# Kernel tuning notes

Measured on AMD Instinct MI355X. Metric: run time of the kernel, lower is better.

The kernel has to match this reference:

```python
import jax, jax.numpy as jnp
import numpy as np

T, B, F, H, P = 256, 512, 256, 512, 12  # seq len, batch, feature_dim, hidden_dim, p_interval


def setup_inputs() -> dict:
    key = jax.random.key(0)
    ks = jax.random.split(key, 9)
    s = 1.0 / np.sqrt(F + H)  # torch Linear default init scale
    def lin(k):
        kw, kb = jax.random.split(k)
        W = jax.random.uniform(kw, (F + H, H), jnp.float32, -s, s)
        b = jax.random.uniform(kb, (H,), jnp.float32, -s, s)
        return W, b
    Wf, bf = lin(ks[0])
    Wi, bi = lin(ks[1])
    Wo, bo = lin(ks[2])
    Wg, bg = lin(ks[3])
    x = jax.random.normal(ks[4], (T, B, F), jnp.float32)
    return {"x": x, "Wf": Wf, "bf": bf, "Wi": Wi, "bi": bi,
            "Wo": Wo, "bo": bo, "Wg": Wg, "bg": bg}


def _slstm(x, Wf, bf, Wi, bi, Wo, bo, Wg, bg):
    Tn, Bn, _ = x.shape
    h0 = jnp.zeros((P, Bn, H), x.dtype)
    # NOTE: original torch code reassigns c to a 2D [B,H] tensor after step 0,
    # so c[t % P] indexes a batch ROW (shape [H]) that broadcasts. At t=0 the
    # slice is all-zeros either way, so carrying a 2D c is exactly faithful.
    c0 = jnp.zeros((Bn, H), x.dtype)

    def step(carry, inp):
        h, c = carry
        x_t, t = inp
        idx = t % P
        xc = jnp.concatenate([x_t, h[idx]], axis=1)  # [B, F+H]
        f = jax.nn.softmax(xc @ Wf + bf, axis=1)
        i = jax.nn.softmax(xc @ Wi + bi, axis=1)
        o = jax.nn.softmax(xc @ Wo + bo, axis=1)
        g = jnp.tanh(xc @ Wg + bg)
        c_new = jnp.tanh(f * c[idx] + i * g)  # c[idx]: row [H], broadcasts over B
        h = h.at[idx].set(o * c_new)
        return (h, c_new), None

    (h, _), _ = jax.lax.scan(step, (h0, c0), (x, jnp.arange(Tn)))
    return h[(Tn - 1) % P]


def reference(x, Wf, bf, Wi, bi, Wo, bo, Wg, bg):
    return _slstm(x, Wf, bf, Wi, bi, Wo, bo, Wg, bg)
```

## Files before the change

kernel.cpp:

```cpp
#include <hip/hip_runtime.h>

typedef unsigned short u16;
typedef unsigned int   u32;

typedef __attribute__((ext_vector_type(8))) short bf16x8;
typedef __attribute__((ext_vector_type(16))) float f32x16;

__device__ __forceinline__ u16 f2bf(float v) {
    u32 u = __float_as_uint(v);
    u32 r = (u + 0x7fffu + ((u >> 16) & 1u)) >> 16;
    return (u16)r;
}
__device__ __forceinline__ float bf2f(u16 h) { return __uint_as_float(((u32)h) << 16); }

__device__ __forceinline__ float ftanh(float x) {
    float e = __expf(2.0f * x);
    return 1.0f - 2.0f * __builtin_amdgcn_rcpf(e + 1.0f);
}

__device__ __forceinline__ void gl2lds16(const void* g, void* l) {
    __builtin_amdgcn_global_load_lds(
        (const __attribute__((address_space(1))) void*)g,
        (__attribute__((address_space(3))) void*)l, 16, 0, 0);
}

__global__ void init_k(u16* __restrict__ hh, u16* __restrict__ hl, float* __restrict__ cb) {
    int i = blockIdx.x * 256 + threadIdx.x;
    hh[i] = 0; hl[i] = 0;
    if (i < 2 * 512) cb[i] = 0.0f;
}

__global__ void pack_wq(const float* __restrict__ Wf, const float* __restrict__ bf_,
                        const float* __restrict__ Wi, const float* __restrict__ bi_,
                        const float* __restrict__ Wo, const float* __restrict__ bo_,
                        const float* __restrict__ Wg, const float* __restrict__ bg_,
                        u16* __restrict__ wq, float* __restrict__ bias4) {
    int idx = blockIdx.x * 256 + threadIdx.x;
    int n = idx / 768, k = idx - n * 768;
    int gate = n >> 9, col = n & 511;
    const float* W = (gate == 0) ? Wf : (gate == 1) ? Wi : (gate == 2) ? Wo : Wg;
    float v = W[k * 512 + col];
    u16 h = f2bf(v);
    u16 l = f2bf(v - bf2f(h));
    size_t base = (size_t)n * 2304;
    if (k < 256) {
        wq[base + k] = h; wq[base + 512 + k] = h; wq[base + 256 + k] = l;
    } else {
        int d = k - 256;
        wq[base + 768 + d] = h; wq[base + 1792 + d] = h; wq[base + 1280 + d] = l;
    }
    if (k == 0) {
        const float* bb = (gate == 0) ? bf_ : (gate == 1) ? bi_ : (gate == 2) ? bo_ : bg_;
        bias4[n] = bb[col];
    }
}

__global__ void split_x(const float* __restrict__ src, u16* __restrict__ oh, u16* __restrict__ ol) {
    int i = blockIdx.x * 256 + threadIdx.x;
    float4 v = ((const float4*)src)[i];
    u16 hx = f2bf(v.x), hy = f2bf(v.y), hz = f2bf(v.z), hw = f2bf(v.w);
    u16 lx = f2bf(v.x - bf2f(hx)), ly = f2bf(v.y - bf2f(hy));
    u16 lz = f2bf(v.z - bf2f(hz)), lw = f2bf(v.w - bf2f(hw));
    uint2 hv; hv.x = (u32)hx | ((u32)hy << 16); hv.y = (u32)hz | ((u32)hw << 16);
    uint2 lv; lv.x = (u32)lx | ((u32)ly << 16); lv.y = (u32)lz | ((u32)lw << 16);
    ((uint2*)oh)[i] = hv;
    ((uint2*)ol)[i] = lv;
}

#define KT 72
__global__ __launch_bounds__(512, 2) void gemm_q(
    const u16* __restrict__ xh, const u16* __restrict__ xl,
    const u16* __restrict__ hh, const u16* __restrict__ hl,
    const u16* __restrict__ wq, const float* __restrict__ bias4,
    float* __restrict__ lg, int Mvalid, int gx) {
    __shared__ __align__(16) u16 smem[57344];

    const int tid = threadIdx.x;
    const int wid = tid >> 6, lane = tid & 63;
    const int l32 = lane & 31, khalf = lane >> 5;
    const int wm = wid >> 2, wn = wid & 3;

    int bm, bn;
    if (gx == 32) { int xcd = blockIdx.x & 7, r = blockIdx.x >> 3; bm = xcd * 4 + (r & 3); bn = r >> 2; }
    else          { bm = blockIdx.x % gx; bn = blockIdx.x / gx; }

    const int rl  = lane >> 2;
    const int bq  = lane & 3;
    const int rlh = rl >> 3;
    const int cA0 = wid;
    const int cA1 = (wid < 4) ? 8 + wid : wid;
    const int cB0 = 2 * wid, cB1 = 2 * wid + 1;

    int arow0 = bm * 192 + cA0 * 16 + rl; if (arow0 >= Mvalid) arow0 = Mvalid - 1;
    int arow1 = bm * 192 + cA1 * 16 + rl; if (arow1 >= Mvalid) arow1 = Mvalid - 1;
    const int ak0 = (bq ^ ((2 * cA0 + rlh) & 3)) * 8;
    const int ak1 = (bq ^ ((2 * cA1 + rlh) & 3)) * 8;
    const size_t brow0 = (size_t)(bn * 256 + cB0 * 16 + rl) * 2304;
    const size_t brow1 = (size_t)(bn * 256 + cB1 * 16 + rl) * 2304;
    const int bk0 = (bq ^ ((2 * cB0 + rlh) & 3)) * 8;
    const int bk1 = (bq ^ ((2 * cB1 + rlh) & 3)) * 8;
    const u32 ldsA0 = (u32)cA0 * 512 + (u32)lane * 8;
    const u32 ldsA1 = (u32)cA1 * 512 + (u32)lane * 8;
    const u32 ldsB0 = (u32)cB0 * 512 + (u32)lane * 8;
    const u32 ldsB1 = (u32)cB1 * 512 + (u32)lane * 8;

#define STAGE(kt_, ao_, bo_) do {                                             \
        int k_ = (kt_); const u16* ab_; int astr_, ako_;                      \
        if (k_ < 24) { ab_ = (k_ >= 16) ? xl : xh; astr_ = 256; ako_ = (k_ & 7) * 32; } \
        else { int sub_ = k_ - 24; ab_ = (sub_ >= 32) ? hl : hh; astr_ = 512; ako_ = (sub_ & 15) * 32; } \
        gl2lds16(ab_ + (size_t)arow0 * astr_ + ako_ + ak0, smem + (ao_) + ldsA0); \
        gl2lds16(ab_ + (size_t)arow1 * astr_ + ako_ + ak1, smem + (ao_) + ldsA1); \
        gl2lds16(wq + brow0 + (size_t)k_ * 32 + bk0, smem + (bo_) + ldsB0);   \
        gl2lds16(wq + brow1 + (size_t)k_ * 32 + bk1, smem + (bo_) + ldsB1);   \
    } while (0)

    const u32 swzr = (u32)(l32 >> 3);
    u32 rowA[3], rowB[2], xk[2];
#pragma unroll
    for (int i = 0; i < 3; ++i) rowA[i] = (u32)(wm * 96 + i * 32 + l32) * 32;
#pragma unroll
    for (int j = 0; j < 2; ++j) rowB[j] = (u32)(wn * 64 + j * 32 + l32) * 32;
#pragma unroll
    for (int ks = 0; ks < 2; ++ks) xk[ks] = (((u32)(ks * 2 + khalf)) ^ swzr) << 3;

    f32x16 acc[3][2];
#pragma unroll
    for (int i = 0; i < 3; ++i)
#pragma unroll
        for (int j = 0; j < 2; ++j)
#pragma unroll
            for (int r = 0; r < 16; ++r) acc[i][j][r] = 0.f;

    bf16x8 s0A0, s0A1, s0A2, s0B0, s0B1;
    bf16x8 s1A0, s1A1, s1A2, s1B0, s1B1;

#define RD(S, ao_, bo_, ks_) do {                                             \
        S##A0 = *(const bf16x8*)(smem + (ao_) + rowA[0] + xk[ks_]);           \
        S##A1 = *(const bf16x8*)(smem + (ao_) + rowA[1] + xk[ks_]);           \
        S##A2 = *(const bf16x8*)(smem + (ao_) + rowA[2] + xk[ks_]);           \
        S##B0 = *(const bf16x8*)(smem + (bo_) + rowB[0] + xk[ks_]);           \
        S##B1 = *(const bf16x8*)(smem + (bo_) + rowB[1] + xk[ks_]);           \
    } while (0)
#define MM(S) do {                                                            \
        __builtin_amdgcn_s_setprio(1);                                        \
        acc[0][0] = __builtin_amdgcn_mfma_f32_32x32x16_bf16(S##A0, S##B0, acc[0][0], 0, 0, 0); \
        acc[0][1] = __builtin_amdgcn_mfma_f32_32x32x16_bf16(S##A0, S##B1, acc[0][1], 0, 0, 0); \
        acc[1][0] = __builtin_amdgcn_mfma_f32_32x32x16_bf16(S##A1, S##B0, acc[1][0], 0, 0, 0); \
        acc[1][1] = __builtin_amdgcn_mfma_f32_32x32x16_bf16(S##A1, S##B1, acc[1][1], 0, 0, 0); \
        acc[2][0] = __builtin_amdgcn_mfma_f32_32x32x16_bf16(S##A2, S##B0, acc[2][0], 0, 0, 0); \
        acc[2][1] = __builtin_amdgcn_mfma_f32_32x32x16_bf16(S##A2, S##B1, acc[2][1], 0, 0, 0); \
        __builtin_amdgcn_s_setprio(0);                                        \
    } while (0)

#define AB(r) ((r) * 6144)
#define BB(r) (24576 + (r) * 8192)

    STAGE(0, AB(0), BB(0));
    STAGE(1, AB(1), BB(1));
    STAGE(2, AB(2), BB(2));
    asm volatile("s_waitcnt vmcnt(4)" ::: "memory");
    asm volatile("s_barrier" ::: "memory");
    __builtin_amdgcn_sched_barrier(0);
    RD(s0, AB(0), BB(0), 0);
    RD(s1, AB(0), BB(0), 1);

#define BODY(kt_, RC, RN, RS) do {                                            \
        if ((kt_) + 3 < KT) STAGE((kt_) + 3, AB(RS), BB(RS));                 \
        MM(s0);                                                               \
        RD(s0, AB(RN), BB(RN), 0);                                            \
        MM(s1);                                                               \
        RD(s1, AB(RN), BB(RN), 1);                                            \
        if ((kt_) + 3 < KT) asm volatile("s_waitcnt vmcnt(4)" ::: "memory");  \
        else                asm volatile("s_waitcnt vmcnt(0)" ::: "memory");  \
        asm volatile("s_barrier" ::: "memory");                               \
        __builtin_amdgcn_sched_barrier(0);                                    \
    } while (0)

#pragma unroll 1
    for (int q = 0; q < 18; ++q) {
        int ktb = q * 4;
        BODY(ktb + 0, 0, 1, 3);
        BODY(ktb + 1, 1, 2, 0);
        BODY(ktb + 2, 2, 3, 1);
        BODY(ktb + 3, 3, 0, 2);
    }
#undef BODY
#undef STAGE
#undef RD
#undef MM
#undef AB
#undef BB

#pragma unroll
    for (int j = 0; j < 2; ++j) {
        int n = bn * 256 + wn * 64 + j * 32 + l32;
        float bv = bias4[n];
#pragma unroll
        for (int i = 0; i < 3; ++i) {
            int rbase = bm * 192 + wm * 96 + i * 32 + 4 * khalf;
#pragma unroll
            for (int r = 0; r < 16; ++r) {
                int row = rbase + (r & 3) + 8 * (r >> 2);
                if (row < Mvalid)
                    lg[(size_t)row * 2048 + n] = acc[i][j][r] + bv;
            }
        }
    }
}

__device__ __forceinline__ void chain_step(const float* __restrict__ lg, int j, int lane, float r[8]) {
    int rowb = (j + 1) % 12;
    const float* base = lg + (size_t)(j * 512 + rowb) * 2048 + lane * 8;
    float f[8], iv[8], g[8];
#pragma unroll
    for (int u = 0; u < 8; ++u) { f[u] = base[u]; iv[u] = base[512 + u]; g[u] = base[1536 + u]; }
    float mf = -1e30f, mi = -1e30f;
#pragma unroll
    for (int u = 0; u < 8; ++u) { mf = fmaxf(mf, f[u]); mi = fmaxf(mi, iv[u]); }
#pragma unroll
    for (int o = 32; o; o >>= 1) { mf = fmaxf(mf, __shfl_xor(mf, o)); mi = fmaxf(mi, __shfl_xor(mi, o)); }
    float sf = 0.f, si = 0.f;
#pragma unroll
    for (int u = 0; u < 8; ++u) {
        f[u] = __expf(f[u] - mf); sf += f[u];
        iv[u] = __expf(iv[u] - mi); si += iv[u];
    }
#pragma unroll
    for (int o = 32; o; o >>= 1) { sf += __shfl_xor(sf, o); si += __shfl_xor(si, o); }
    float rf = __builtin_amdgcn_rcpf(sf), ri = __builtin_amdgcn_rcpf(si);
#pragma unroll
    for (int u = 0; u < 8; ++u) {
        float gg = ftanh(g[u]);
        r[u] = ftanh(f[u] * rf * r[u] + iv[u] * ri * gg);
    }
}

__global__ __launch_bounds__(256) void gates_k(
    const float* __restrict__ lg, float* __restrict__ cb,
    u16* __restrict__ hh, u16* __restrict__ hl,
    float* __restrict__ out, int t0, int S, int rd, int wr) {
    __shared__ float rsh[512];
    const int widx = threadIdx.x >> 6, lane = threadIdx.x & 63;
    const int s = (S - 1) - (blockIdx.x >> 7);
    const int b = (blockIdx.x & 127) * 4 + widx;
    const int t = t0 + s;

    if (widx == 0) {
        float r[8];
#pragma unroll
        for (int u = 0; u < 8; ++u) r[u] = cb[rd * 512 + lane * 8 + u];
        for (int j = 0; j < s; ++j) chain_step(lg, j, lane, r);
#pragma unroll
        for (int u = 0; u < 8; ++u) rsh[lane * 8 + u] = r[u];
        if ((int)blockIdx.x == 127 && t0 + S < 256) {
            chain_step(lg, S - 1, lane, r);
#pragma unroll
            for (int u = 0; u < 8; ++u) cb[wr * 512 + lane * 8 + u] = r[u];
        }
    }
    __syncthreads();

    const float* row = lg + (size_t)(s * 512 + b) * 2048 + lane * 8;
    float f[8], iv[8], ov[8], g[8];
#pragma unroll
    for (int u = 0; u < 8; ++u) {
        f[u] = row[u]; iv[u] = row[512 + u]; ov[u] = row[1024 + u]; g[u] = row[1536 + u];
    }
    float mf = -1e30f, mi = -1e30f, mo = -1e30f;
#pragma unroll
    for (int u = 0; u < 8; ++u) { mf = fmaxf(mf, f[u]); mi = fmaxf(mi, iv[u]); mo = fmaxf(mo, ov[u]); }
#pragma unroll
    for (int o = 32; o; o >>= 1) {
        mf = fmaxf(mf, __shfl_xor(mf, o));
        mi = fmaxf(mi, __shfl_xor(mi, o));
        mo = fmaxf(mo, __shfl_xor(mo, o));
    }
    float sf = 0.f, si = 0.f, so = 0.f;
#pragma unroll
    for (int u = 0; u < 8; ++u) {
        f[u] = __expf(f[u] - mf); sf += f[u];
        iv[u] = __expf(iv[u] - mi); si += iv[u];
        ov[u] = __expf(ov[u] - mo); so += ov[u];
    }
#pragma unroll
    for (int o = 32; o; o >>= 1) {
        sf += __shfl_xor(sf, o); si += __shfl_xor(si, o); so += __shfl_xor(so, o);
    }
    float rf = __builtin_amdgcn_rcpf(sf), ri = __builtin_amdgcn_rcpf(si), ro = __builtin_amdgcn_rcpf(so);
    float hout[8];
#pragma unroll
    for (int u = 0; u < 8; ++u) {
        float rr = rsh[lane * 8 + u];
        float gg = ftanh(g[u]);
        float cv = ftanh(f[u] * rf * rr + iv[u] * ri * gg);
        hout[u] = ov[u] * ro * cv;
    }
    u32 hhp[4], hlp[4];
#pragma unroll
    for (int u = 0; u < 4; ++u) {
        u16 h0 = f2bf(hout[2 * u]), h1 = f2bf(hout[2 * u + 1]);
        u16 l0 = f2bf(hout[2 * u] - bf2f(h0)), l1 = f2bf(hout[2 * u + 1] - bf2f(h1));
        hhp[u] = (u32)h0 | ((u32)h1 << 16);
        hlp[u] = (u32)l0 | ((u32)l1 << 16);
    }
    size_t hb = ((size_t)(s * 512 + b)) * 512 + lane * 8;
    *(uint4*)&hh[hb] = make_uint4(hhp[0], hhp[1], hhp[2], hhp[3]);
    *(uint4*)&hl[hb] = make_uint4(hlp[0], hlp[1], hlp[2], hlp[3]);
    if (t == 255) {
        float* op = out + (size_t)b * 512 + lane * 8;
#pragma unroll
        for (int u = 0; u < 8; ++u) op[u] = hout[u];
    }
}

extern "C" void kernel_launch(void* const* d_in, const int* in_sizes, int n_in,
                              void* d_out, int out_size, void* d_ws, size_t ws_size,
                              hipStream_t stream) {
    const float* x   = (const float*)d_in[0];
    const float* Wf  = (const float*)d_in[1];
    const float* bf_ = (const float*)d_in[2];
    const float* Wi  = (const float*)d_in[3];
    const float* bi_ = (const float*)d_in[4];
    const float* Wo  = (const float*)d_in[5];
    const float* bo_ = (const float*)d_in[6];
    const float* Wg  = (const float*)d_in[7];
    const float* bg_ = (const float*)d_in[8];
    float* out = (float*)d_out;

    char* p = (char*)d_ws;
    u16* xh  = (u16*)p; p += 134217728;
    u16* xl  = (u16*)p; p += 134217728;
    u16* wq  = (u16*)p; p += 9437184;
    u16* hh  = (u16*)p; p += 6291456;
    u16* hl  = (u16*)p; p += 6291456;
    float* bias4 = (float*)p; p += 8192;
    float* cb    = (float*)p; p += 4096;
    float* lg    = (float*)p; p += 50331648;

    init_k<<<12288, 256, 0, stream>>>(hh, hl, cb);
    pack_wq<<<6144, 256, 0, stream>>>(Wf, bf_, Wi, bi_, Wo, bo_, Wg, bg_, wq, bias4);
    split_x<<<32768, 256, 0, stream>>>(x, xh, xl);

    for (int blk = 0; blk < 22; ++blk) {
        int t0 = blk * 12;
        int S = (256 - t0 >= 12) ? 12 : (256 - t0);
        int M = S * 512;
        int gx = (M + 191) / 192;
        gemm_q<<<gx * 8, 512, 0, stream>>>(
            xh + (size_t)t0 * 512 * 256, xl + (size_t)t0 * 512 * 256,
            hh, hl, wq, bias4, lg, M, gx);
        gates_k<<<S * 128, 256, 0, stream>>>(lg, cb, hh, hl, out, t0, S, blk & 1, (blk + 1) & 1);
    }
}
```

Before: 2.142 ms.

## Load A operand directly from global into registers, bypassing LDS staging

The A operand (x/h bf16 splits) is now read straight from global memory into MFMA registers with a one-step register double buffer. Only B (weights) is still staged through LDS, which shrinks shared memory from 112KB to 64KB per block. The aim is to cut LDS traffic and LDS footprint. The cost is more VGPR pressure, uncoalesced-ish 16B global loads per lane, and hand-tuned vmcnt waits that must match the new load counts.

```diff
diff --git a/kernel.cpp b/kernel.cpp
--- a/kernel.cpp
+++ b/kernel.cpp
@@ -73,7 +73,7 @@
     const u16* __restrict__ hh, const u16* __restrict__ hl,
     const u16* __restrict__ wq, const float* __restrict__ bias4,
     float* __restrict__ lg, int Mvalid, int gx) {
-    __shared__ __align__(16) u16 smem[57344];
+    __shared__ __align__(16) u16 smem[32768];
 
     const int tid = threadIdx.x;
     const int wid = tid >> 6, lane = tid & 63;
@@ -87,41 +87,56 @@
     const int rl  = lane >> 2;
     const int bq  = lane & 3;
     const int rlh = rl >> 3;
-    const int cA0 = wid;
-    const int cA1 = (wid < 4) ? 8 + wid : wid;
     const int cB0 = 2 * wid, cB1 = 2 * wid + 1;
-
-    int arow0 = bm * 192 + cA0 * 16 + rl; if (arow0 >= Mvalid) arow0 = Mvalid - 1;
-    int arow1 = bm * 192 + cA1 * 16 + rl; if (arow1 >= Mvalid) arow1 = Mvalid - 1;
-    const int ak0 = (bq ^ ((2 * cA0 + rlh) & 3)) * 8;
-    const int ak1 = (bq ^ ((2 * cA1 + rlh) & 3)) * 8;
     const size_t brow0 = (size_t)(bn * 256 + cB0 * 16 + rl) * 2304;
     const size_t brow1 = (size_t)(bn * 256 + cB1 * 16 + rl) * 2304;
     const int bk0 = (bq ^ ((2 * cB0 + rlh) & 3)) * 8;
     const int bk1 = (bq ^ ((2 * cB1 + rlh) & 3)) * 8;
-    const u32 ldsA0 = (u32)cA0 * 512 + (u32)lane * 8;
-    const u32 ldsA1 = (u32)cA1 * 512 + (u32)lane * 8;
     const u32 ldsB0 = (u32)cB0 * 512 + (u32)lane * 8;
     const u32 ldsB1 = (u32)cB1 * 512 + (u32)lane * 8;
 
-#define STAGE(kt_, ao_, bo_) do {                                             \
-        int k_ = (kt_); const u16* ab_; int astr_, ako_;                      \
-        if (k_ < 24) { ab_ = (k_ >= 16) ? xl : xh; astr_ = 256; ako_ = (k_ & 7) * 32; } \
-        else { int sub_ = k_ - 24; ab_ = (sub_ >= 32) ? hl : hh; astr_ = 512; ako_ = (sub_ & 15) * 32; } \
-        gl2lds16(ab_ + (size_t)arow0 * astr_ + ako_ + ak0, smem + (ao_) + ldsA0); \
-        gl2lds16(ab_ + (size_t)arow1 * astr_ + ako_ + ak1, smem + (ao_) + ldsA1); \
-        gl2lds16(wq + brow0 + (size_t)k_ * 32 + bk0, smem + (bo_) + ldsB0);   \
-        gl2lds16(wq + brow1 + (size_t)k_ * 32 + bk1, smem + (bo_) + ldsB1);   \
-    } while (0)
-
-    const u32 swzr = (u32)(l32 >> 3);
-    u32 rowA[3], rowB[2], xk[2];
-#pragma unroll
-    for (int i = 0; i < 3; ++i) rowA[i] = (u32)(wm * 96 + i * 32 + l32) * 32;
+#define BB(r) ((r) * 8192)
+#define STAGE_B(kt_, bo_) do {                                                \
+        gl2lds16(wq + brow0 + (size_t)(kt_) * 32 + bk0, smem + (bo_) + ldsB0);\
+        gl2lds16(wq + brow1 + (size_t)(kt_) * 32 + bk1, smem + (bo_) + ldsB1);\
+    } while (0)
+
+    u32 offx[3], offh[3];
+#pragma unroll
+    for (int i = 0; i < 3; ++i) {
+        int row = bm * 192 + wm * 96 + i * 32 + l32;
+        if (row >= Mvalid) row = Mvalid - 1;
+        offx[i] = (u32)row * 256 + (u32)khalf * 8;
+        offh[i] = (u32)row * 512 + (u32)khalf * 8;
+    }
+
+#define LOADA(kt_, DST) do {                                                  \
+        int k_ = (kt_);                                                       \
+        if (k_ < 24) {                                                        \
+            const u16* bp_ = (k_ >= 16) ? xl : xh; int ko_ = (k_ & 7) * 32;   \
+            DST[0] = *(const bf16x8*)(bp_ + ko_ + offx[0]);                   \
+            DST[1] = *(const bf16x8*)(bp_ + ko_ + offx[1]);                   \
+            DST[2] = *(const bf16x8*)(bp_ + ko_ + offx[2]);                   \
+            DST[3] = *(const bf16x8*)(bp_ + ko_ + offx[0] + 16);              \
+            DST[4] = *(const bf16x8*)(bp_ + ko_ + offx[1] + 16);              \
+            DST[5] = *(const bf16x8*)(bp_ + ko_ + offx[2] + 16);              \
+        } else {                                                              \
+            int sub_ = k_ - 24;                                               \
+            const u16* bp_ = (sub_ >= 32) ? hl : hh; int ko_ = (sub_ & 15) * 32; \
+            DST[0] = *(const bf16x8*)(bp_ + ko_ + offh[0]);                   \
+            DST[1] = *(const bf16x8*)(bp_ + ko_ + offh[1]);                   \
+            DST[2] = *(const bf16x8*)(bp_ + ko_ + offh[2]);                   \
+            DST[3] = *(const bf16x8*)(bp_ + ko_ + offh[0] + 16);              \
+            DST[4] = *(const bf16x8*)(bp_ + ko_ + offh[1] + 16);              \
+            DST[5] = *(const bf16x8*)(bp_ + ko_ + offh[2] + 16);              \
+        }                                                                     \
+    } while (0)
+
+    u32 rowB[2], xk[2];
 #pragma unroll
     for (int j = 0; j < 2; ++j) rowB[j] = (u32)(wn * 64 + j * 32 + l32) * 32;
 #pragma unroll
-    for (int ks = 0; ks < 2; ++ks) xk[ks] = (((u32)(ks * 2 + khalf)) ^ swzr) << 3;
+    for (int ks = 0; ks < 2; ++ks) xk[ks] = (((u32)(ks * 2 + khalf)) ^ (u32)(l32 >> 3)) << 3;
 
     f32x16 acc[3][2];
 #pragma unroll
@@ -131,64 +146,71 @@
 #pragma unroll
             for (int r = 0; r < 16; ++r) acc[i][j][r] = 0.f;
 
-    bf16x8 s0A0, s0A1, s0A2, s0B0, s0B1;
-    bf16x8 s1A0, s1A1, s1A2, s1B0, s1B1;
-
-#define RD(S, ao_, bo_, ks_) do {                                             \
-        S##A0 = *(const bf16x8*)(smem + (ao_) + rowA[0] + xk[ks_]);           \
-        S##A1 = *(const bf16x8*)(smem + (ao_) + rowA[1] + xk[ks_]);           \
-        S##A2 = *(const bf16x8*)(smem + (ao_) + rowA[2] + xk[ks_]);           \
-        S##B0 = *(const bf16x8*)(smem + (bo_) + rowB[0] + xk[ks_]);           \
-        S##B1 = *(const bf16x8*)(smem + (bo_) + rowB[1] + xk[ks_]);           \
-    } while (0)
-#define MM(S) do {                                                            \
+    bf16x8 aP[6], aQ[6];
+    bf16x8 b00, b01, b10, b11;
+
+#define RD_B0(bo_) do {                                                       \
+        b00 = *(const bf16x8*)(smem + (bo_) + rowB[0] + xk[0]);               \
+        b01 = *(const bf16x8*)(smem + (bo_) + rowB[1] + xk[0]);               \
+    } while (0)
+#define RD_B1(bo_) do {                                                       \
+        b10 = *(const bf16x8*)(smem + (bo_) + rowB[0] + xk[1]);               \
+        b11 = *(const bf16x8*)(smem + (bo_) + rowB[1] + xk[1]);               \
+    } while (0)
+#define MMK(AS, k0, B0_, B1_) do {                                            \
         __builtin_amdgcn_s_setprio(1);                                        \
-        acc[0][0] = __builtin_amdgcn_mfma_f32_32x32x16_bf16(S##A0, S##B0, acc[0][0], 0, 0, 0); \
-        acc[0][1] = __builtin_amdgcn_mfma_f32_32x32x16_bf16(S##A0, S##B1, acc[0][1], 0, 0, 0); \
-        acc[1][0] = __builtin_amdgcn_mfma_f32_32x32x16_bf16(S##A1, S##B0, acc[1][0], 0, 0, 0); \
-        acc[1][1] = __builtin_amdgcn_mfma_f32_32x32x16_bf16(S##A1, S##B1, acc[1][1], 0, 0, 0); \
-        acc[2][0] = __builtin_amdgcn_mfma_f32_32x32x16_bf16(S##A2, S##B0, acc[2][0], 0, 0, 0); \
-        acc[2][1] = __builtin_amdgcn_mfma_f32_32x32x16_bf16(S##A2, S##B1, acc[2][1], 0, 0, 0); \
+        acc[0][0] = __builtin_amdgcn_mfma_f32_32x32x16_bf16(AS[(k0)+0], B0_, acc[0][0], 0, 0, 0); \
+        acc[0][1] = __builtin_amdgcn_mfma_f32_32x32x16_bf16(AS[(k0)+0], B1_, acc[0][1], 0, 0, 0); \
+        acc[1][0] = __builtin_amdgcn_mfma_f32_32x32x16_bf16(AS[(k0)+1], B0_, acc[1][0], 0, 0, 0); \
+        acc[1][1] = __builtin_amdgcn_mfma_f32_32x32x16_bf16(AS[(k0)+1], B1_, acc[1][1], 0, 0, 0); \
+        acc[2][0] = __builtin_amdgcn_mfma_f32_32x32x16_bf16(AS[(k0)+2], B0_, acc[2][0], 0, 0, 0); \
+        acc[2][1] = __builtin_amdgcn_mfma_f32_32x32x16_bf16(AS[(k0)+2], B1_, acc[2][1], 0, 0, 0); \
         __builtin_amdgcn_s_setprio(0);                                        \
     } while (0)
 
-#define AB(r) ((r) * 6144)
-#define BB(r) (24576 + (r) * 8192)
-
-    STAGE(0, AB(0), BB(0));
-    STAGE(1, AB(1), BB(1));
-    STAGE(2, AB(2), BB(2));
-    asm volatile("s_waitcnt vmcnt(4)" ::: "memory");
+    LOADA(0, aP);
+    __builtin_amdgcn_sched_barrier(0);
+    STAGE_B(0, BB(0)); STAGE_B(1, BB(1)); STAGE_B(2, BB(2));
+    asm volatile("s_waitcnt vmcnt(2)" ::: "memory");
     asm volatile("s_barrier" ::: "memory");
     __builtin_amdgcn_sched_barrier(0);
-    RD(s0, AB(0), BB(0), 0);
-    RD(s1, AB(0), BB(0), 1);
-
-#define BODY(kt_, RC, RN, RS) do {                                            \
-        if ((kt_) + 3 < KT) STAGE((kt_) + 3, AB(RS), BB(RS));                 \
-        MM(s0);                                                               \
-        RD(s0, AB(RN), BB(RN), 0);                                            \
-        MM(s1);                                                               \
-        RD(s1, AB(RN), BB(RN), 1);                                            \
-        if ((kt_) + 3 < KT) asm volatile("s_waitcnt vmcnt(4)" ::: "memory");  \
-        else                asm volatile("s_waitcnt vmcnt(0)" ::: "memory");  \
-        asm volatile("s_barrier" ::: "memory");                               \
+    RD_B0(BB(0)); RD_B1(BB(0));
+
+#define BODY(kt_, RN, RS, CUR, NXT) do {                                      \
+        asm volatile("s_waitcnt vmcnt(2)" ::: "memory");   \
+        if ((kt_) + 1 < KT) LOADA((kt_) + 1, NXT);                \
         __builtin_amdgcn_sched_barrier(0);                                    \
+        if ((kt_) + 3 < KT) STAGE_B((kt_) + 3, BB(RS));           \
+        __builtin_amdgcn_sched_barrier(0);                                    \
+        MMK(CUR, 0, b00, b01);                                                \
+        if ((kt_) + 1 < KT) RD_B0(BB(RN));                                    \
+        MMK(CUR, 3, b10, b11);                                                \
+        if ((kt_) + 1 < KT) RD_B1(BB(RN));                                    \
+        if ((kt_) < KT - 3) {                                                 \
+            asm volatile("s_waitcnt vmcnt(8)" ::: "memory"); \
+            asm volatile("s_barrier" ::: "memory");                           \
+            __builtin_amdgcn_sched_barrier(0);                                \
+        } else if ((kt_) < KT - 1) {                                          \
+            asm volatile("s_waitcnt vmcnt(6)" ::: "memory");                  \
+            asm volatile("s_barrier" ::: "memory");                           \
+            __builtin_amdgcn_sched_barrier(0);                                \
+        }                                                                     \
     } while (0)
 
 #pragma unroll 1
     for (int q = 0; q < 18; ++q) {
         int ktb = q * 4;
-        BODY(ktb + 0, 0, 1, 3);
-        BODY(ktb + 1, 1, 2, 0);
-        BODY(ktb + 2, 2, 3, 1);
-        BODY(ktb + 3, 3, 0, 2);
+        BODY(ktb + 0, 1, 3, aP, aQ);
+        BODY(ktb + 1, 2, 0, aQ, aP);
+        BODY(ktb + 2, 3, 1, aP, aQ);
+        BODY(ktb + 3, 0, 2, aQ, aP);
     }
 #undef BODY
-#undef STAGE
-#undef RD
-#undef MM
-#undef AB
+#undef STAGE_B
+#undef LOADA
+#undef RD_B0
+#undef RD_B1
+#undef MMK
 #undef BB
 
 #pragma unroll
```

Result: slower. 3.565 ms (+66.4%).
